# Kernel optimization log

Hardware: AMD Instinct MI355X
Metric: run time of the kernel (lower is better)

Reference implementation:

```python
import jax, jax.numpy as jnp
import numpy as np

N_NODES = 50000
N_EDGES = 800000
N_GRAPHS = 512
HEADS = 4
HDIM = 64
NEG_SLOPE = 0.2


def setup_inputs() -> dict:
    key = jax.random.key(0)
    ks = jax.random.split(key, 16)
    x = jax.random.normal(ks[0], (N_NODES, 128), dtype=jnp.float32)
    edge_index = jax.random.randint(ks[1], (2, N_EDGES), 0, N_NODES, dtype=jnp.int64)
    batch = jnp.sort(jax.random.randint(ks[2], (N_NODES,), 0, N_GRAPHS, dtype=jnp.int64))
    def glorot(k, shape):
        fan = shape[0] + shape[-1]
        return jax.random.normal(k, shape, dtype=jnp.float32) * jnp.sqrt(2.0 / fan)
    return {
        "x": x, "edge_index": edge_index, "batch": batch,
        "W1": glorot(ks[3], (128, 256)), "a_src1": glorot(ks[4], (HEADS, HDIM)), "a_dst1": glorot(ks[5], (HEADS, HDIM)), "b1": jnp.zeros((256,), jnp.float32),
        "W2": glorot(ks[6], (256, 256)), "a_src2": glorot(ks[7], (HEADS, HDIM)), "a_dst2": glorot(ks[8], (HEADS, HDIM)), "b2": jnp.zeros((256,), jnp.float32),
        "W3": glorot(ks[9], (256, 256)), "a_src3": glorot(ks[10], (HEADS, HDIM)), "a_dst3": glorot(ks[11], (HEADS, HDIM)), "b3": jnp.zeros((256,), jnp.float32),
        "fc_W": glorot(ks[12], (256, 1)), "fc_b": jnp.zeros((1,), jnp.float32),
    }


def gat_layer(x, W, a_src, a_dst, b, src, dst):
    # x: [N, F_in] -> h: [N, H, C]
    N = x.shape[0]
    h = (x @ W).reshape(N, HEADS, HDIM)
    alpha_s = jnp.sum(h * a_src[None], axis=-1)  # [N, H]
    alpha_d = jnp.sum(h * a_dst[None], axis=-1)  # [N, H]
    logits = jax.nn.leaky_relu(alpha_s[src] + alpha_d[dst], NEG_SLOPE)  # [E, H]
    # segment softmax over destination nodes
    m = jax.ops.segment_max(logits, dst, num_segments=N)  # [N, H]
    e = jnp.exp(logits - m[dst])
    denom = jax.ops.segment_sum(e, dst, num_segments=N)
    alpha = e / denom[dst]  # [E, H]
    msg = h[src] * alpha[:, :, None]  # [E, H, C]
    out = jax.ops.segment_sum(msg, dst, num_segments=N).reshape(N, HEADS * HDIM)
    return out + b


def reference(x, edge_index, batch, W1, a_src1, a_dst1, b1, W2, a_src2, a_dst2, b2, W3, a_src3, a_dst3, b3, fc_W, fc_b):
    N = x.shape[0]
    loop = jnp.arange(N, dtype=edge_index.dtype)
    # PyG GATConv adds self-loops by default
    src = jnp.concatenate([edge_index[0], loop])
    dst = jnp.concatenate([edge_index[1], loop])
    h = gat_layer(x, W1, a_src1, a_dst1, b1, src, dst)
    h = gat_layer(h, W2, a_src2, a_dst2, b2, src, dst)
    h = gat_layer(h, W3, a_src3, a_dst3, b3, src, dst)
    pooled = jax.ops.segment_sum(h, batch, num_segments=N_GRAPHS)  # [G, 256]
    return pooled @ fc_W + fc_b
```

## Files before the change

### kernel.cpp

```cpp
#include <hip/hip_runtime.h>
#include <hip/hip_bf16.h>
#include <math.h>

#define NN 50000
#define NE 800000
#define ET (NE + NN)
#define NG 512
#define NEG 0.2f

typedef __attribute__((ext_vector_type(8))) short bf16x8;
typedef __attribute__((ext_vector_type(4))) float f32x4;

__device__ inline unsigned f2o(float f) {
    unsigned b = __float_as_uint(f);
    return (b & 0x80000000u) ? ~b : (b | 0x80000000u);
}
__device__ inline float o2f(unsigned u) {
    return (u & 0x80000000u) ? __uint_as_float(u ^ 0x80000000u) : __uint_as_float(~u);
}
__device__ inline unsigned short f2b(float f) {
    unsigned u = __float_as_uint(f);
    u += 0x7fffu + ((u >> 16) & 1u);
    return (unsigned short)(u >> 16);
}
__device__ inline float b2f(unsigned short b) {
    return __uint_as_float(((unsigned)b) << 16);
}

__global__ __launch_bounds__(256) void split_weights(const float* __restrict__ W1,
        const float* __restrict__ W2, const float* __restrict__ W3,
        unsigned short* __restrict__ WTh, unsigned short* __restrict__ WTl) {
    int tid = blockIdx.x * 256 + threadIdx.x;
    const float* W; int K, n, k, base;
    if (tid < 32768)       { W = W1; K = 128; base = 0;     int i = tid;          n = i >> 7; k = i & 127; }
    else if (tid < 98304)  { W = W2; K = 256; base = 32768; int i = tid - 32768;  n = i >> 8; k = i & 255; }
    else if (tid < 163840) { W = W3; K = 256; base = 98304; int i = tid - 98304;  n = i >> 8; k = i & 255; }
    else return;
    float w = W[k * 256 + n];
    unsigned short hi = f2b(w);
    float lo = w - b2f(hi);
    WTh[base + n * K + k] = hi;
    WTl[base + n * K + k] = f2b(lo);
}

template<int K, int AFP32>
__global__ __launch_bounds__(256) void gemm_mfma(const float* __restrict__ Af,
        const unsigned short* __restrict__ Ahi, const unsigned short* __restrict__ Alo,
        const unsigned short* __restrict__ Bhi, const unsigned short* __restrict__ Blo,
        unsigned short* __restrict__ h,
        const float* __restrict__ a_src, const float* __restrict__ a_dst,
        float* __restrict__ as_, float* __restrict__ ad_) {
    __shared__ unsigned short AsH[128][40], AsL[128][40], BsH[128][40], BsL[128][40];
    const int t = threadIdx.x;
    const int mb = blockIdx.x >> 1, nb = blockIdx.x & 1;
    const int m0 = mb * 128, n0 = nb * 128;
    const int wid = t >> 6, lane = t & 63;
    const int wr = wid >> 1, wc = wid & 1;
    const int lr = lane & 15, lg = lane >> 4;

    f32x4 acc[4][4];
    #pragma unroll
    for (int mi = 0; mi < 4; ++mi)
        #pragma unroll
        for (int ni = 0; ni < 4; ++ni)
            acc[mi][ni] = (f32x4){0.f, 0.f, 0.f, 0.f};

    for (int k0 = 0; k0 < K; k0 += 32) {
        __syncthreads();
        #pragma unroll
        for (int cc = 0; cc < 2; ++cc) {
            int c = t + cc * 256;
            int row = c >> 2, kc = c & 3;
            int gr = m0 + row; if (gr >= NN) gr = NN - 1;
            if (AFP32) {
                const float* pa = Af + (size_t)gr * K + k0 + kc * 8;
                float4 f0 = *(const float4*)pa;
                float4 f1 = *(const float4*)(pa + 4);
                union { unsigned short u[8]; uint4 v; } th, tl;
                float fs[8] = {f0.x, f0.y, f0.z, f0.w, f1.x, f1.y, f1.z, f1.w};
                #pragma unroll
                for (int j = 0; j < 8; ++j) {
                    unsigned short hv = f2b(fs[j]);
                    th.u[j] = hv;
                    tl.u[j] = f2b(fs[j] - b2f(hv));
                }
                *(uint4*)&AsH[row][kc * 8] = th.v;
                *(uint4*)&AsL[row][kc * 8] = tl.v;
            } else {
                *(uint4*)&AsH[row][kc * 8] = *(const uint4*)(Ahi + (size_t)gr * K + k0 + kc * 8);
                *(uint4*)&AsL[row][kc * 8] = *(const uint4*)(Alo + (size_t)gr * K + k0 + kc * 8);
            }
            *(uint4*)&BsH[row][kc * 8] = *(const uint4*)(Bhi + (size_t)(n0 + row) * K + k0 + kc * 8);
            *(uint4*)&BsL[row][kc * 8] = *(const uint4*)(Blo + (size_t)(n0 + row) * K + k0 + kc * 8);
        }
        __syncthreads();

        bf16x8 ah[4], al[4];
        #pragma unroll
        for (int mi = 0; mi < 4; ++mi) {
            int ra = wr * 64 + mi * 16 + lr;
            ah[mi] = *(const bf16x8*)&AsH[ra][lg * 8];
            al[mi] = *(const bf16x8*)&AsL[ra][lg * 8];
        }
        #pragma unroll
        for (int ni = 0; ni < 4; ++ni) {
            int rb = wc * 64 + ni * 16 + lr;
            bf16x8 bh = *(const bf16x8*)&BsH[rb][lg * 8];
            bf16x8 bl = *(const bf16x8*)&BsL[rb][lg * 8];
            #pragma unroll
            for (int mi = 0; mi < 4; ++mi) {
                acc[mi][ni] = __builtin_amdgcn_mfma_f32_16x16x32_bf16(bh, ah[mi], acc[mi][ni], 0, 0, 0);
                acc[mi][ni] = __builtin_amdgcn_mfma_f32_16x16x32_bf16(bh, al[mi], acc[mi][ni], 0, 0, 0);
                acc[mi][ni] = __builtin_amdgcn_mfma_f32_16x16x32_bf16(bl, ah[mi], acc[mi][ni], 0, 0, 0);
            }
        }
    }

    const int head = nb * 2 + wc;
    const int ncol0 = n0 + wc * 64;
    float4 asv[4], adv[4];
    #pragma unroll
    for (int ni = 0; ni < 4; ++ni) {
        asv[ni] = *(const float4*)&a_src[head * 64 + ni * 16 + lg * 4];
        adv[ni] = *(const float4*)&a_dst[head * 64 + ni * 16 + lg * 4];
    }
    #pragma unroll
    for (int mi = 0; mi < 4; ++mi) {
        float ps = 0.f, pd = 0.f;
        #pragma unroll
        for (int ni = 0; ni < 4; ++ni) {
            ps = fmaf(acc[mi][ni][0], asv[ni].x, ps); pd = fmaf(acc[mi][ni][0], adv[ni].x, pd);
            ps = fmaf(acc[mi][ni][1], asv[ni].y, ps); pd = fmaf(acc[mi][ni][1], adv[ni].y, pd);
            ps = fmaf(acc[mi][ni][2], asv[ni].z, ps); pd = fmaf(acc[mi][ni][2], adv[ni].z, pd);
            ps = fmaf(acc[mi][ni][3], asv[ni].w, ps); pd = fmaf(acc[mi][ni][3], adv[ni].w, pd);
        }
        ps += __shfl_xor(ps, 16, 64); ps += __shfl_xor(ps, 32, 64);
        pd += __shfl_xor(pd, 16, 64); pd += __shfl_xor(pd, 32, 64);
        int row = m0 + wr * 64 + mi * 16 + lr;
        if (row < NN) {
            #pragma unroll
            for (int ni = 0; ni < 4; ++ni) {
                ushort4 hv = {f2b(acc[mi][ni][0]), f2b(acc[mi][ni][1]),
                              f2b(acc[mi][ni][2]), f2b(acc[mi][ni][3])};
                *(ushort4*)&h[(size_t)row * 256 + ncol0 + ni * 16 + lg * 4] = hv;
            }
            if (lane < 16) { as_[row * 4 + head] = ps; ad_[row * 4 + head] = pd; }
        }
    }
}

__global__ void gmax_init(unsigned* gmax) {
    if (threadIdx.x < 4) gmax[threadIdx.x] = 0u;
}
__global__ __launch_bounds__(256) void gmax_reduce(const float* __restrict__ as_,
                                                   unsigned* gmax) {
    float m0 = -1e30f, m1 = -1e30f, m2 = -1e30f, m3 = -1e30f;
    for (int n = blockIdx.x * 256 + threadIdx.x; n < NN; n += gridDim.x * 256) {
        float4 a = *(const float4*)&as_[n * 4];
        m0 = fmaxf(m0, a.x); m1 = fmaxf(m1, a.y);
        m2 = fmaxf(m2, a.z); m3 = fmaxf(m3, a.w);
    }
    #pragma unroll
    for (int off = 32; off; off >>= 1) {
        m0 = fmaxf(m0, __shfl_xor(m0, off, 64));
        m1 = fmaxf(m1, __shfl_xor(m1, off, 64));
        m2 = fmaxf(m2, __shfl_xor(m2, off, 64));
        m3 = fmaxf(m3, __shfl_xor(m3, off, 64));
    }
    __shared__ float sm[4][4];
    int lane = threadIdx.x & 63, w = threadIdx.x >> 6;
    if (lane == 0) { sm[w][0] = m0; sm[w][1] = m1; sm[w][2] = m2; sm[w][3] = m3; }
    __syncthreads();
    if (threadIdx.x == 0) {
        #pragma unroll
        for (int hd = 0; hd < 4; ++hd) {
            float mm = fmaxf(fmaxf(sm[0][hd], sm[1][hd]), fmaxf(sm[2][hd], sm[3][hd]));
            atomicMax(&gmax[hd], f2o(mm));
        }
    }
}

__global__ void init_counts(int* counts, int* esrc_pad) {
    int i = blockIdx.x * 256 + threadIdx.x;
    if (i < NN) counts[i] = 1;
    if (i < 16) esrc_pad[i] = 0;
}
__global__ void count_kernel(const int* __restrict__ dst, int* counts) {
    int e = blockIdx.x * 256 + threadIdx.x;
    if (e < NE) atomicAdd(&counts[dst[e]], 1);
}
__global__ __launch_bounds__(1024) void scan_kernel(const int* __restrict__ counts,
                                                    int* row_ptr, int* cursor) {
    __shared__ int sm[1024];
    const int i = threadIdx.x;
    const int CH = (NN + 1023) / 1024;
    int base = i * CH;
    int s = 0;
    for (int j = 0; j < CH; ++j) { int idx = base + j; if (idx < NN) s += counts[idx]; }
    sm[i] = s; __syncthreads();
    for (int off = 1; off < 1024; off <<= 1) {
        int v = (i >= off) ? sm[i - off] : 0;
        __syncthreads();
        sm[i] += v;
        __syncthreads();
    }
    int run = sm[i] - s;
    for (int j = 0; j < CH; ++j) {
        int idx = base + j;
        if (idx < NN) { row_ptr[idx] = run; cursor[idx] = run; run += counts[idx]; }
    }
    if (i == 1023) row_ptr[NN] = ET;
}
__global__ void scatter_kernel(const int* __restrict__ src, const int* __restrict__ dst,
                               int* cursor, int* esrc) {
    int e = blockIdx.x * 256 + threadIdx.x;
    if (e < NE) {
        int p = atomicAdd(&cursor[dst[e]], 1);
        esrc[p] = src[e];
    } else if (e < ET) {
        int n = e - NE;
        int p = atomicAdd(&cursor[n], 1);
        esrc[p] = n;
    }
}

#define EDGE(ae, he)                                                           \
    {                                                                          \
        float t_ = (ae) + adn; t_ = t_ > 0.f ? t_ : NEG * t_;                  \
        float w_ = __expf(t_ - g); lsum += w_;                                 \
        acc.x = fmaf(w_, b2f((he).x), acc.x);                                  \
        acc.y = fmaf(w_, b2f((he).y), acc.y);                                  \
        acc.z = fmaf(w_, b2f((he).z), acc.z);                                  \
        acc.w = fmaf(w_, b2f((he).w), acc.w);                                  \
    }

template<int FINAL>
__global__ __launch_bounds__(256) void agg_kernel(const unsigned short* __restrict__ h,
        const float* __restrict__ as_, const float* __restrict__ ad_,
        const unsigned* __restrict__ gmax,
        const int* __restrict__ row_ptr, const int* __restrict__ esrc,
        const float* __restrict__ bias,
        unsigned short* __restrict__ ohi, unsigned short* __restrict__ olo,
        float* __restrict__ out,
        const int* __restrict__ batch, const float* __restrict__ fcW) {
    int n = blockIdx.x * 4 + (threadIdx.x >> 6);
    int lane = threadIdx.x & 63;
    if (n >= NN) return;
    const int head = lane >> 4;
    const int c4 = lane * 4;
    int s0 = row_ptr[n], s1 = row_ptr[n + 1];
    float adn = ad_[n * 4 + head];
    float g = o2f(gmax[head]) + adn; g = g > 0.f ? g : NEG * g;
    float lsum = 0.f;
    float4 acc = {0.f, 0.f, 0.f, 0.f};

    int i = s0;
    int iA0 = esrc[i],     iA1 = esrc[i + 1], iA2 = esrc[i + 2], iA3 = esrc[i + 3];
    int iB0 = esrc[i + 4], iB1 = esrc[i + 5], iB2 = esrc[i + 6], iB3 = esrc[i + 7];
    float aA0 = as_[iA0 * 4 + head], aA1 = as_[iA1 * 4 + head];
    float aA2 = as_[iA2 * 4 + head], aA3 = as_[iA3 * 4 + head];
    ushort4 hA0 = *(const ushort4*)&h[(long)iA0 * 256 + c4];
    ushort4 hA1 = *(const ushort4*)&h[(long)iA1 * 256 + c4];
    ushort4 hA2 = *(const ushort4*)&h[(long)iA2 * 256 + c4];
    ushort4 hA3 = *(const ushort4*)&h[(long)iA3 * 256 + c4];

    while (i + 8 <= s1) {
        int iC0 = esrc[i + 8], iC1 = esrc[i + 9], iC2 = esrc[i + 10], iC3 = esrc[i + 11];
        float aB0 = as_[iB0 * 4 + head], aB1 = as_[iB1 * 4 + head];
        float aB2 = as_[iB2 * 4 + head], aB3 = as_[iB3 * 4 + head];
        ushort4 hB0 = *(const ushort4*)&h[(long)iB0 * 256 + c4];
        ushort4 hB1 = *(const ushort4*)&h[(long)iB1 * 256 + c4];
        ushort4 hB2 = *(const ushort4*)&h[(long)iB2 * 256 + c4];
        ushort4 hB3 = *(const ushort4*)&h[(long)iB3 * 256 + c4];
        EDGE(aA0, hA0); EDGE(aA1, hA1); EDGE(aA2, hA2); EDGE(aA3, hA3);
        iB0 = iC0; iB1 = iC1; iB2 = iC2; iB3 = iC3;
        aA0 = aB0; aA1 = aB1; aA2 = aB2; aA3 = aB3;
        hA0 = hB0; hA1 = hB1; hA2 = hB2; hA3 = hB3;
        i += 4;
    }
    if (i + 4 <= s1) {
        EDGE(aA0, hA0); EDGE(aA1, hA1); EDGE(aA2, hA2); EDGE(aA3, hA3);
        i += 4;
    }
    for (; i < s1; ++i) {
        int s = esrc[i];
        float a = as_[s * 4 + head];
        ushort4 hv = *(const ushort4*)&h[(long)s * 256 + c4];
        EDGE(a, hv);
    }

    float rl = 1.f / lsum;
    float4 bv = *(const float4*)&bias[c4];
    float4 o = {fmaf(acc.x, rl, bv.x), fmaf(acc.y, rl, bv.y),
                fmaf(acc.z, rl, bv.z), fmaf(acc.w, rl, bv.w)};
    if (!FINAL) {
        ushort4 vh = {f2b(o.x), f2b(o.y), f2b(o.z), f2b(o.w)};
        ushort4 vl = {f2b(o.x - b2f(vh.x)), f2b(o.y - b2f(vh.y)),
                      f2b(o.z - b2f(vh.z)), f2b(o.w - b2f(vh.w))};
        *(ushort4*)&ohi[(long)n * 256 + c4] = vh;
        *(ushort4*)&olo[(long)n * 256 + c4] = vl;
    } else {
        float4 fw = *(const float4*)&fcW[c4];
        float sd = o.x * fw.x + o.y * fw.y + o.z * fw.z + o.w * fw.w;
        #pragma unroll
        for (int off = 32; off; off >>= 1) sd += __shfl_xor(sd, off, 64);
        if (lane == 0) atomicAdd(&out[batch[n]], sd);
    }
}

__global__ void out_init(const float* __restrict__ fc_b, float* out) {
    int i = blockIdx.x * 256 + threadIdx.x;
    if (i < NG) out[i] = fc_b[0];
}

extern "C" void kernel_launch(void* const* d_in, const int* in_sizes, int n_in,
                              void* d_out, int out_size, void* d_ws, size_t ws_size,
                              hipStream_t stream) {
    const float* x      = (const float*)d_in[0];
    const int*   ei     = (const int*)d_in[1];
    const int*   batch  = (const int*)d_in[2];
    const float* W1     = (const float*)d_in[3];
    const float* as1    = (const float*)d_in[4];
    const float* ad1    = (const float*)d_in[5];
    const float* b1     = (const float*)d_in[6];
    const float* W2     = (const float*)d_in[7];
    const float* as2    = (const float*)d_in[8];
    const float* ad2    = (const float*)d_in[9];
    const float* b2     = (const float*)d_in[10];
    const float* W3     = (const float*)d_in[11];
    const float* as3    = (const float*)d_in[12];
    const float* ad3    = (const float*)d_in[13];
    const float* b3     = (const float*)d_in[14];
    const float* fcW    = (const float*)d_in[15];
    const float* fcb    = (const float*)d_in[16];
    const int* esrc_in = ei;
    const int* edst_in = ei + NE;

    char* ws = (char*)d_ws;
    size_t off = 0;
    unsigned short* hB  = (unsigned short*)(ws + off); off += (size_t)NN * 256 * 2;
    unsigned short* ohi = (unsigned short*)(ws + off); off += (size_t)NN * 256 * 2;
    unsigned short* olo = (unsigned short*)(ws + off); off += (size_t)NN * 256 * 2;
    unsigned short* WTh = (unsigned short*)(ws + off); off += 163840 * 2;
    unsigned short* WTl = (unsigned short*)(ws + off); off += 163840 * 2;
    float* aS    = (float*)(ws + off); off += (size_t)NN * 4 * 4;
    float* aD    = (float*)(ws + off); off += (size_t)NN * 4 * 4;
    int* counts  = (int*)(ws + off);   off += (size_t)NN * 4;
    int* cursor  = (int*)(ws + off);   off += (size_t)NN * 4;
    int* row_ptr = (int*)(ws + off);   off += (size_t)(NN + 1) * 4 + 12;
    unsigned* gmax = (unsigned*)(ws + off); off += 16;
    int* esrc    = (int*)(ws + off);   off += (size_t)(ET + 16) * 4;
    float* out   = (float*)d_out;

    init_counts<<<(NN + 255) / 256, 256, 0, stream>>>(counts, esrc + ET);
    count_kernel<<<(NE + 255) / 256, 256, 0, stream>>>(edst_in, counts);
    scan_kernel<<<1, 1024, 0, stream>>>(counts, row_ptr, cursor);
    scatter_kernel<<<(ET + 255) / 256, 256, 0, stream>>>(esrc_in, edst_in, cursor, esrc);
    split_weights<<<640, 256, 0, stream>>>(W1, W2, W3, WTh, WTl);

    const int GEMM_GRID = ((NN + 127) / 128) * 2;
    const int NODE_GRID = (NN + 3) / 4;

    gmax_init<<<1, 64, 0, stream>>>(gmax);
    gemm_mfma<128, 1><<<GEMM_GRID, 256, 0, stream>>>(x, nullptr, nullptr, WTh, WTl, hB, as1, ad1, aS, aD);
    gmax_reduce<<<128, 256, 0, stream>>>(aS, gmax);
    agg_kernel<0><<<NODE_GRID, 256, 0, stream>>>(hB, aS, aD, gmax, row_ptr, esrc, b1, ohi, olo, nullptr, nullptr, nullptr);
    gmax_init<<<1, 64, 0, stream>>>(gmax);
    gemm_mfma<256, 0><<<GEMM_GRID, 256, 0, stream>>>(nullptr, ohi, olo, WTh + 32768, WTl + 32768, hB, as2, ad2, aS, aD);
    gmax_reduce<<<128, 256, 0, stream>>>(aS, gmax);
    agg_kernel<0><<<NODE_GRID, 256, 0, stream>>>(hB, aS, aD, gmax, row_ptr, esrc, b2, ohi, olo, nullptr, nullptr, nullptr);
    gmax_init<<<1, 64, 0, stream>>>(gmax);
    gemm_mfma<256, 0><<<GEMM_GRID, 256, 0, stream>>>(nullptr, ohi, olo, WTh + 98304, WTl + 98304, hB, as3, ad3, aS, aD);
    gmax_reduce<<<128, 256, 0, stream>>>(aS, gmax);
    out_init<<<(NG + 255) / 256, 256, 0, stream>>>(fcb, out);
    agg_kernel<1><<<NODE_GRID, 256, 0, stream>>>(hB, aS, aD, gmax, row_ptr, esrc, b3, nullptr, nullptr, out, batch, fcW);
}
```

Baseline: 625.9 us.

## Fuse head-max reduction into GEMM epilogue and split node edges across two waves

```diff
diff --git a/kernel.cpp b/kernel.cpp
--- a/kernel.cpp
+++ b/kernel.cpp
@@ -5,6 +5,7 @@
 #define NN 50000
 #define NE 800000
 #define ET (NE + NN)
+#define EP (ET + 40)
 #define NG 512
 #define NEG 0.2f
 
@@ -49,7 +50,8 @@
         const unsigned short* __restrict__ Bhi, const unsigned short* __restrict__ Blo,
         unsigned short* __restrict__ h,
         const float* __restrict__ a_src, const float* __restrict__ a_dst,
-        float* __restrict__ as_, float* __restrict__ ad_) {
+        float* __restrict__ as_, float* __restrict__ ad_,
+        unsigned* __restrict__ gmax) {
     __shared__ unsigned short AsH[128][40], AsL[128][40], BsH[128][40], BsL[128][40];
     const int t = threadIdx.x;
     const int mb = blockIdx.x >> 1, nb = blockIdx.x & 1;
@@ -124,6 +126,7 @@
         asv[ni] = *(const float4*)&a_src[head * 64 + ni * 16 + lg * 4];
         adv[ni] = *(const float4*)&a_dst[head * 64 + ni * 16 + lg * 4];
     }
+    float pmax = -1e30f;
     #pragma unroll
     for (int mi = 0; mi < 4; ++mi) {
         float ps = 0.f, pd = 0.f;
@@ -136,6 +139,7 @@
         }
         ps += __shfl_xor(ps, 16, 64); ps += __shfl_xor(ps, 32, 64);
         pd += __shfl_xor(pd, 16, 64); pd += __shfl_xor(pd, 32, 64);
+        pmax = fmaxf(pmax, ps);
         int row = m0 + wr * 64 + mi * 16 + lr;
         if (row < NN) {
             #pragma unroll
@@ -147,43 +151,18 @@
             if (lane < 16) { as_[row * 4 + head] = ps; ad_[row * 4 + head] = pd; }
         }
     }
-}
-
-__global__ void gmax_init(unsigned* gmax) {
-    if (threadIdx.x < 4) gmax[threadIdx.x] = 0u;
-}
-__global__ __launch_bounds__(256) void gmax_reduce(const float* __restrict__ as_,
-                                                   unsigned* gmax) {
-    float m0 = -1e30f, m1 = -1e30f, m2 = -1e30f, m3 = -1e30f;
-    for (int n = blockIdx.x * 256 + threadIdx.x; n < NN; n += gridDim.x * 256) {
-        float4 a = *(const float4*)&as_[n * 4];
-        m0 = fmaxf(m0, a.x); m1 = fmaxf(m1, a.y);
-        m2 = fmaxf(m2, a.z); m3 = fmaxf(m3, a.w);
-    }
-    #pragma unroll
-    for (int off = 32; off; off >>= 1) {
-        m0 = fmaxf(m0, __shfl_xor(m0, off, 64));
-        m1 = fmaxf(m1, __shfl_xor(m1, off, 64));
-        m2 = fmaxf(m2, __shfl_xor(m2, off, 64));
-        m3 = fmaxf(m3, __shfl_xor(m3, off, 64));
-    }
-    __shared__ float sm[4][4];
-    int lane = threadIdx.x & 63, w = threadIdx.x >> 6;
-    if (lane == 0) { sm[w][0] = m0; sm[w][1] = m1; sm[w][2] = m2; sm[w][3] = m3; }
-    __syncthreads();
-    if (threadIdx.x == 0) {
-        #pragma unroll
-        for (int hd = 0; hd < 4; ++hd) {
-            float mm = fmaxf(fmaxf(sm[0][hd], sm[1][hd]), fmaxf(sm[2][hd], sm[3][hd]));
-            atomicMax(&gmax[hd], f2o(mm));
-        }
-    }
-}
-
-__global__ void init_counts(int* counts, int* esrc_pad) {
+    pmax = fmaxf(pmax, __shfl_xor(pmax, 1, 64));
+    pmax = fmaxf(pmax, __shfl_xor(pmax, 2, 64));
+    pmax = fmaxf(pmax, __shfl_xor(pmax, 4, 64));
+    pmax = fmaxf(pmax, __shfl_xor(pmax, 8, 64));
+    if (lane == 0) atomicMax(&gmax[head], f2o(pmax));
+}
+
+__global__ void init_counts(int* counts, int* esrc_pad, unsigned* gmax) {
     int i = blockIdx.x * 256 + threadIdx.x;
     if (i < NN) counts[i] = 1;
-    if (i < 16) esrc_pad[i] = 0;
+    if (i < 40) esrc_pad[i] = 0;
+    if (i < 12) gmax[i] = 0u;
 }
 __global__ void count_kernel(const int* __restrict__ dst, int* counts) {
     int e = blockIdx.x * 256 + threadIdx.x;
@@ -243,68 +222,93 @@
         unsigned short* __restrict__ ohi, unsigned short* __restrict__ olo,
         float* __restrict__ out,
         const int* __restrict__ batch, const float* __restrict__ fcW) {
-    int n = blockIdx.x * 4 + (threadIdx.x >> 6);
-    int lane = threadIdx.x & 63;
-    if (n >= NN) return;
+    __shared__ float part[2][64][5];
+    const int wid = threadIdx.x >> 6;
+    const int lane = threadIdx.x & 63;
+    const int slot = wid >> 1;
+    const int half = wid & 1;
+    int n = blockIdx.x * 2 + slot;
     const int head = lane >> 4;
     const int c4 = lane * 4;
     int s0 = row_ptr[n], s1 = row_ptr[n + 1];
+    int deg = s1 - s0;
+    int h0 = (deg + 1) >> 1;
+    int e0 = s0 + (half ? h0 : 0);
+    int e1 = half ? s1 : s0 + h0;
     float adn = ad_[n * 4 + head];
     float g = o2f(gmax[head]) + adn; g = g > 0.f ? g : NEG * g;
     float lsum = 0.f;
     float4 acc = {0.f, 0.f, 0.f, 0.f};
 
-    int i = s0;
-    int iA0 = esrc[i],     iA1 = esrc[i + 1], iA2 = esrc[i + 2], iA3 = esrc[i + 3];
-    int iB0 = esrc[i + 4], iB1 = esrc[i + 5], iB2 = esrc[i + 6], iB3 = esrc[i + 7];
-    float aA0 = as_[iA0 * 4 + head], aA1 = as_[iA1 * 4 + head];
-    float aA2 = as_[iA2 * 4 + head], aA3 = as_[iA3 * 4 + head];
-    ushort4 hA0 = *(const ushort4*)&h[(long)iA0 * 256 + c4];
-    ushort4 hA1 = *(const ushort4*)&h[(long)iA1 * 256 + c4];
-    ushort4 hA2 = *(const ushort4*)&h[(long)iA2 * 256 + c4];
-    ushort4 hA3 = *(const ushort4*)&h[(long)iA3 * 256 + c4];
-
-    while (i + 8 <= s1) {
-        int iC0 = esrc[i + 8], iC1 = esrc[i + 9], iC2 = esrc[i + 10], iC3 = esrc[i + 11];
-        float aB0 = as_[iB0 * 4 + head], aB1 = as_[iB1 * 4 + head];
-        float aB2 = as_[iB2 * 4 + head], aB3 = as_[iB3 * 4 + head];
-        ushort4 hB0 = *(const ushort4*)&h[(long)iB0 * 256 + c4];
-        ushort4 hB1 = *(const ushort4*)&h[(long)iB1 * 256 + c4];
-        ushort4 hB2 = *(const ushort4*)&h[(long)iB2 * 256 + c4];
-        ushort4 hB3 = *(const ushort4*)&h[(long)iB3 * 256 + c4];
-        EDGE(aA0, hA0); EDGE(aA1, hA1); EDGE(aA2, hA2); EDGE(aA3, hA3);
-        iB0 = iC0; iB1 = iC1; iB2 = iC2; iB3 = iC3;
-        aA0 = aB0; aA1 = aB1; aA2 = aB2; aA3 = aB3;
-        hA0 = hB0; hA1 = hB1; hA2 = hB2; hA3 = hB3;
-        i += 4;
-    }
-    if (i + 4 <= s1) {
-        EDGE(aA0, hA0); EDGE(aA1, hA1); EDGE(aA2, hA2); EDGE(aA3, hA3);
-        i += 4;
-    }
-    for (; i < s1; ++i) {
-        int s = esrc[i];
-        float a = as_[s * 4 + head];
-        ushort4 hv = *(const ushort4*)&h[(long)s * 256 + c4];
-        EDGE(a, hv);
-    }
-
-    float rl = 1.f / lsum;
-    float4 bv = *(const float4*)&bias[c4];
-    float4 o = {fmaf(acc.x, rl, bv.x), fmaf(acc.y, rl, bv.y),
-                fmaf(acc.z, rl, bv.z), fmaf(acc.w, rl, bv.w)};
-    if (!FINAL) {
-        ushort4 vh = {f2b(o.x), f2b(o.y), f2b(o.z), f2b(o.w)};
-        ushort4 vl = {f2b(o.x - b2f(vh.x)), f2b(o.y - b2f(vh.y)),
-                      f2b(o.z - b2f(vh.z)), f2b(o.w - b2f(vh.w))};
-        *(ushort4*)&ohi[(long)n * 256 + c4] = vh;
-        *(ushort4*)&olo[(long)n * 256 + c4] = vl;
-    } else {
-        float4 fw = *(const float4*)&fcW[c4];
-        float sd = o.x * fw.x + o.y * fw.y + o.z * fw.z + o.w * fw.w;
-        #pragma unroll
-        for (int off = 32; off; off >>= 1) sd += __shfl_xor(sd, off, 64);
-        if (lane == 0) atomicAdd(&out[batch[n]], sd);
+    if (e0 < e1) {
+        int i = e0;
+        int iA0 = esrc[i],     iA1 = esrc[i + 1], iA2 = esrc[i + 2], iA3 = esrc[i + 3];
+        int iB0 = esrc[i + 4], iB1 = esrc[i + 5], iB2 = esrc[i + 6], iB3 = esrc[i + 7];
+        float aA0 = as_[iA0 * 4 + head], aA1 = as_[iA1 * 4 + head];
+        float aA2 = as_[iA2 * 4 + head], aA3 = as_[iA3 * 4 + head];
+        ushort4 hA0 = *(const ushort4*)&h[(long)iA0 * 256 + c4];
+        ushort4 hA1 = *(const ushort4*)&h[(long)iA1 * 256 + c4];
+        ushort4 hA2 = *(const ushort4*)&h[(long)iA2 * 256 + c4];
+        ushort4 hA3 = *(const ushort4*)&h[(long)iA3 * 256 + c4];
+
+        while (i + 8 <= e1) {
+            int iC0 = esrc[i + 8], iC1 = esrc[i + 9], iC2 = esrc[i + 10], iC3 = esrc[i + 11];
+            float aB0 = as_[iB0 * 4 + head], aB1 = as_[iB1 * 4 + head];
+            float aB2 = as_[iB2 * 4 + head], aB3 = as_[iB3 * 4 + head];
+            ushort4 hB0 = *(const ushort4*)&h[(long)iB0 * 256 + c4];
+            ushort4 hB1 = *(const ushort4*)&h[(long)iB1 * 256 + c4];
+            ushort4 hB2 = *(const ushort4*)&h[(long)iB2 * 256 + c4];
+            ushort4 hB3 = *(const ushort4*)&h[(long)iB3 * 256 + c4];
+            EDGE(aA0, hA0); EDGE(aA1, hA1); EDGE(aA2, hA2); EDGE(aA3, hA3);
+            iB0 = iC0; iB1 = iC1; iB2 = iC2; iB3 = iC3;
+            aA0 = aB0; aA1 = aB1; aA2 = aB2; aA3 = aB3;
+            hA0 = hB0; hA1 = hB1; hA2 = hB2; hA3 = hB3;
+            i += 4;
+        }
+        if (i + 4 <= e1) {
+            EDGE(aA0, hA0); EDGE(aA1, hA1); EDGE(aA2, hA2); EDGE(aA3, hA3);
+            i += 4;
+        }
+        for (; i < e1; ++i) {
+            int s = esrc[i];
+            float a = as_[s * 4 + head];
+            ushort4 hv = *(const ushort4*)&h[(long)s * 256 + c4];
+            EDGE(a, hv);
+        }
+    }
+
+    if (half) {
+        part[slot][lane][0] = lsum;
+        part[slot][lane][1] = acc.x;
+        part[slot][lane][2] = acc.y;
+        part[slot][lane][3] = acc.z;
+        part[slot][lane][4] = acc.w;
+    }
+    __syncthreads();
+    if (half == 0) {
+        lsum  += part[slot][lane][0];
+        acc.x += part[slot][lane][1];
+        acc.y += part[slot][lane][2];
+        acc.z += part[slot][lane][3];
+        acc.w += part[slot][lane][4];
+
+        float rl = 1.f / lsum;
+        float4 bv = *(const float4*)&bias[c4];
+        float4 o = {fmaf(acc.x, rl, bv.x), fmaf(acc.y, rl, bv.y),
+                    fmaf(acc.z, rl, bv.z), fmaf(acc.w, rl, bv.w)};
+        if (!FINAL) {
+            ushort4 vh = {f2b(o.x), f2b(o.y), f2b(o.z), f2b(o.w)};
+            ushort4 vl = {f2b(o.x - b2f(vh.x)), f2b(o.y - b2f(vh.y)),
+                          f2b(o.z - b2f(vh.z)), f2b(o.w - b2f(vh.w))};
+            *(ushort4*)&ohi[(long)n * 256 + c4] = vh;
+            *(ushort4*)&olo[(long)n * 256 + c4] = vl;
+        } else {
+            float4 fw = *(const float4*)&fcW[c4];
+            float sd = o.x * fw.x + o.y * fw.y + o.z * fw.z + o.w * fw.w;
+            #pragma unroll
+            for (int off = 32; off; off >>= 1) sd += __shfl_xor(sd, off, 64);
+            if (lane == 0) atomicAdd(&out[batch[n]], sd);
+        }
     }
 }
 
@@ -348,30 +352,24 @@
     int* counts  = (int*)(ws + off);   off += (size_t)NN * 4;
     int* cursor  = (int*)(ws + off);   off += (size_t)NN * 4;
     int* row_ptr = (int*)(ws + off);   off += (size_t)(NN + 1) * 4 + 12;
-    unsigned* gmax = (unsigned*)(ws + off); off += 16;
-    int* esrc    = (int*)(ws + off);   off += (size_t)(ET + 16) * 4;
+    unsigned* gmax = (unsigned*)(ws + off); off += 48;
+    int* esrc    = (int*)(ws + off);   off += (size_t)EP * 4;
     float* out   = (float*)d_out;
 
-    init_counts<<<(NN + 255) / 256, 256, 0, stream>>>(counts, esrc + ET);
+    init_counts<<<(NN + 255) / 256, 256, 0, stream>>>(counts, esrc + ET, gmax);
     count_kernel<<<(NE + 255) / 256, 256, 0, stream>>>(edst_in, counts);
     scan_kernel<<<1, 1024, 0, stream>>>(counts, row_ptr, cursor);
     scatter_kernel<<<(ET + 255) / 256, 256, 0, stream>>>(esrc_in, edst_in, cursor, esrc);
     split_weights<<<640, 256, 0, stream>>>(W1, W2, W3, WTh, WTl);
 
     const int GEMM_GRID = ((NN + 127) / 128) * 2;
-    const int NODE_GRID = (NN + 3) / 4;
-
-    gmax_init<<<1, 64, 0, stream>>>(gmax);
-    gemm_mfma<128, 1><<<GEMM_GRID, 256, 0, stream>>>(x, nullptr, nullptr, WTh, WTl, hB, as1, ad1, aS, aD);
-    gmax_reduce<<<128, 256, 0, stream>>>(aS, gmax);
-    agg_kernel<0><<<NODE_GRID, 256, 0, stream>>>(hB, aS, aD, gmax, row_ptr, esrc, b1, ohi, olo, nullptr, nullptr, nullptr);
-    gmax_init<<<1, 64, 0, stream>>>(gmax);
-    gemm_mfma<256, 0><<<GEMM_GRID, 256, 0, stream>>>(nullptr, ohi, olo, WTh + 32768, WTl + 32768, hB, as2, ad2, aS, aD);
-    gmax_reduce<<<128, 256, 0, stream>>>(aS, gmax);
-    agg_kernel<0><<<NODE_GRID, 256, 0, stream>>>(hB, aS, aD, gmax, row_ptr, esrc, b2, ohi, olo, nullptr, nullptr, nullptr);
-    gmax_init<<<1, 64, 0, stream>>>(gmax);
-    gemm_mfma<256, 0><<<GEMM_GRID, 256, 0, stream>>>(nullptr, ohi, olo, WTh + 98304, WTl + 98304, hB, as3, ad3, aS, aD);
-    gmax_reduce<<<128, 256, 0, stream>>>(aS, gmax);
+    const int NODE_GRID2 = NN / 2;
+
+    gemm_mfma<128, 1><<<GEMM_GRID, 256, 0, stream>>>(x, nullptr, nullptr, WTh, WTl, hB, as1, ad1, aS, aD, gmax);
+    agg_kernel<0><<<NODE_GRID2, 256, 0, stream>>>(hB, aS, aD, gmax, row_ptr, esrc, b1, ohi, olo, nullptr, nullptr, nullptr);
+    gemm_mfma<256, 0><<<GEMM_GRID, 256, 0, stream>>>(nullptr, ohi, olo, WTh + 32768, WTl + 32768, hB, as2, ad2, aS, aD, gmax + 4);
+    agg_kernel<0><<<NODE_GRID2, 256, 0, stream>>>(hB, aS, aD, gmax + 4, row_ptr, esrc, b2, ohi, olo, nullptr, nullptr, nullptr);
+    gemm_mfma<256, 0><<<GEMM_GRID, 256, 0, stream>>>(nullptr, ohi, olo, WTh + 98304, WTl + 98304, hB, as3, ad3, aS, aD, gmax + 8);
     out_init<<<(NG + 255) / 256, 256, 0, stream>>>(fcb, out);
-    agg_kernel<1><<<NODE_GRID, 256, 0, stream>>>(hB, aS, aD, gmax, row_ptr, esrc, b3, nullptr, nullptr, out, batch, fcW);
-}
+    agg_kernel<1><<<NODE_GRID2, 256, 0, stream>>>(hB, aS, aD, gmax + 8, row_ptr, esrc, b3, nullptr, nullptr, out, batch, fcW);
+}
```

New measurement: 702.7 us. +12.3%, slower.
